# Kernel optimization log

Hardware: AMD Instinct MI355X
Metric: run time of the kernel (lower is better)

Reference implementation:

```python
import jax, jax.numpy as jnp
import numpy as np

ALPHA = 0.2      # LeakyReLU negative slope (alpha)
KNN = 5          # knn_num / cluster_num in get_center_1
M = 5            # m in get_dc
CC = 3           # cluster_centers
NEG = -9e15
EPS = 9e-15

def _pdist(x):
    sq = jnp.sum(x * x, axis=1)
    d2 = sq[:, None] + sq[None, :] - 2.0 * (x @ x.T)
    return jnp.sqrt(jnp.maximum(d2, 0.0))

def _cdist(x, c):
    d2 = jnp.sum(x * x, 1)[:, None] + jnp.sum(c * c, 1)[None, :] - 2.0 * (x @ c.T)
    return jnp.sqrt(jnp.maximum(d2, 0.0))

def _kmeans(x, k=CC, iters=10):
    # deterministic stand-in for sklearn KMeans(n_clusters=3, init='k-means++'):
    # farthest-point init + fixed Lloyd iterations
    c0 = x[0]
    d = jnp.sum((x - c0) ** 2, 1)
    c1 = x[jnp.argmax(d)]
    d = jnp.minimum(d, jnp.sum((x - c1) ** 2, 1))
    c2 = x[jnp.argmax(d)]
    centers = jnp.stack([c0, c1, c2])
    def step(c, _):
        assign = jnp.argmin(_cdist(x, c), axis=1)
        oh = jax.nn.one_hot(assign, k, dtype=x.dtype)
        newc = (oh.T @ x) / jnp.maximum(oh.sum(0), 1.0)[:, None]
        return newc, None
    centers, _ = jax.lax.scan(step, centers, None, length=iters)
    return centers

def _gravity(h):
    # get_center_1: fully built from detached tensors in the original -> stop_gradient
    x = jax.lax.stop_gradient(h)
    n = x.shape[0]
    z = _pdist(x)                                 # [n, n] pairwise distances
    negv, loc = jax.lax.top_k(-z, M + 1)          # M+1 smallest distances per row
    dc = jnp.mean(-negv[:, 1])                    # mean nearest-neighbor distance
    knn_idx = loc[:, 1:KNN + 1]                   # 5-NN (excluding self)
    rows = jnp.arange(n)[:, None]
    knn_vals = jnp.take_along_axis(z, knn_idx, axis=1)
    ori = jnp.zeros_like(z).at[rows, knn_idx].set(knn_vals)   # dists only at 5-NN
    nearest = jnp.take_along_axis(ori, loc[:, 1:2], axis=1)
    safe = jnp.where(ori != 0, ori, 1.0)
    ori = jnp.where(ori != 0, dc * nearest / (safe * safe), ori)
    # replicate the source's global flat-index mask (index = arange(size).reshape)
    flat = jnp.arange(n * n).reshape(n, n)
    mincol = jnp.min(jnp.argsort(ori, axis=1)[:, -KNN:], axis=1, keepdims=True)
    ori = jnp.where(flat >= mincol, 0.0, ori) - EPS
    centers = _kmeans(x)
    d1 = _cdist(x, centers)                       # [n, 3] node->center distances
    nearest1 = d1[:, 1:2]                         # cupy wrap: (i*3+1) % 3 == 1
    safe1 = jnp.where(d1 != 0, d1, 1.0)
    d1 = jnp.where(d1 != 0, dc * nearest1 / (safe1 * safe1), d1) - EPS
    z3 = jnp.full((CC, CC), NEG, dtype=x.dtype)
    top = jnp.concatenate([ori, d1], axis=1)
    bot = jnp.concatenate([d1.T, z3], axis=1)
    return jnp.concatenate([top, bot], axis=0)    # [(n+3), (n+3)]

def _forward(h, W, a, t1, t2):
    n, fin = h.shape
    fout = W.shape[1]
    Wh = h @ W
    s = Wh @ a[:fout] + (Wh @ a[fout:]).T         # [n, n]
    e = jnp.where(s > 0, s, ALPHA * s)            # LeakyReLU attention logits
    g = _gravity(h)
    att = jnp.concatenate([
        jnp.concatenate([e, t1], axis=1),
        jnp.concatenate([t2, jnp.zeros((CC, CC), h.dtype)], axis=1),
    ], axis=0)                                    # [(n+3), (n+3)]
    att = jax.nn.softmax(g @ att, axis=1)         # dropout omitted (eval mode)
    h_pad = jnp.concatenate([h, jnp.zeros((CC, fin), h.dtype)], axis=0)
    out = att @ (h_pad @ W)                       # [(n+3), fout]
    return jax.nn.elu(out)                        # concat=True

def setup_inputs():
    key = jax.random.key(0)
    k = jax.random.split(key, 5)
    N, FIN, FOUT = 4096, 512, 64
    gain = 1.414
    limW = gain * np.sqrt(6.0 / (FIN + FOUT))
    lima = gain * np.sqrt(6.0 / (2 * FOUT + 1))
    return {
        "h": jax.random.normal(k[0], (N, FIN), jnp.float32),
        "adj": jnp.zeros((N, N), jnp.float32),   # accepted but unused by forward
        "W": jax.random.uniform(k[1], (FIN, FOUT), jnp.float32, -limW, limW),
        "a": jax.random.uniform(k[2], (2 * FOUT, 1), jnp.float32, -lima, lima),
        "t1": jax.random.normal(k[3], (N, CC), jnp.float32),
        "t2": jax.random.normal(k[4], (CC, N), jnp.float32),
    }

def reference(h, adj, W, a, t1, t2):
    return _forward(h, W, a, t1, t2)
```

## Files before the change

### kernel.cpp

```cpp
#include <hip/hip_runtime.h>
#include <hip/hip_bf16.h>
#include <math.h>

#define NPTS 4096
#define FIN 512
#define FOUT 64
#define SCALE 4194304.0f
#define INVSCALE 2.384185791015625e-7f

typedef __attribute__((ext_vector_type(8))) short bf16x8;
typedef __attribute__((ext_vector_type(4))) float f32x4;
typedef unsigned long long ull;

static __device__ __forceinline__ unsigned short bfbits(float x) {
  __hip_bfloat16 b = __float2bfloat16(x);
  return *reinterpret_cast<unsigned short*>(&b);
}

static __device__ __forceinline__ float wsum64(float v) {
  #pragma unroll
  for (int mm = 1; mm < 64; mm <<= 1) v += __shfl_xor(v, mm);
  return v;
}

static __device__ __forceinline__ int aloadi(int* p) {
  return __hip_atomic_load(p, __ATOMIC_RELAXED, __HIP_MEMORY_SCOPE_AGENT);
}
static __device__ __forceinline__ ull aloadu(ull* p) {
  return __hip_atomic_load(p, __ATOMIC_RELAXED, __HIP_MEMORY_SCOPE_AGENT);
}

__global__ __launch_bounds__(256) void k_prep(const float* __restrict__ h,
    const float* __restrict__ W, __hip_bfloat16* __restrict__ xb,
    float* __restrict__ sq, int* __restrict__ m1, __hip_bfloat16* __restrict__ WbT,
    ull* __restrict__ accZ, int* __restrict__ cntZ, int* __restrict__ barZ) {
  int bid = blockIdx.x, t = threadIdx.x;
  if (bid >= 1026) {
    int idx = (bid - 1026) * 256 + t;
    #pragma unroll
    for (int s = 0; s < 10; ++s) accZ[s * 1536 + idx] = 0ull;
    if (idx < 40) cntZ[idx] = 0;
    if (idx < 32) barZ[idx] = 0;
    return;
  }
  if (bid >= 1024) {
    int base = (bid - 1024) * 16384;
    for (int rep = 0; rep < 64; ++rep) {
      int e = base + rep * 256 + t;
      int n = e >> 9, k = e & 511;
      WbT[e] = __float2bfloat16(W[k * FOUT + n]);
    }
    return;
  }
  int lane = t & 63, wid = t >> 6;
  int row = bid * 4 + wid;
  const float4* hr = (const float4*)(h + (size_t)row * FIN);
  float4 a = hr[lane], b = hr[64 + lane];
  ushort4 pa = { bfbits(a.x), bfbits(a.y), bfbits(a.z), bfbits(a.w) };
  ushort4 pb = { bfbits(b.x), bfbits(b.y), bfbits(b.z), bfbits(b.w) };
  *(ushort4*)(xb + (size_t)row * FIN + 4 * lane) = pa;
  *(ushort4*)(xb + (size_t)row * FIN + 256 + 4 * lane) = pb;
  float s = a.x*a.x + a.y*a.y + a.z*a.z + a.w*a.w
          + b.x*b.x + b.y*b.y + b.z*b.z + b.w*b.w;
  s = wsum64(s);
  if (lane == 0) { sq[row] = s; m1[row] = 0x7F800000; }
}

__device__ __forceinline__ void gram_role(const __hip_bfloat16* __restrict__ xb,
    const float* __restrict__ sq, int* __restrict__ m1, int gb, char* smem) {
  bool act = threadIdx.x < 256;
  int tid = threadIdx.x;
  int lane = tid & 63, wid = tid >> 6;
  int b = gb, I = 0;
  while (b >= 32 - I) { b -= 32 - I; ++I; }
  int J = I + b;
  char* As = smem;
  char* Bs = smem + 16384;

  int R0 = I * 128, C0 = J * 128;
  int rowBase = (wid >> 1) * 64;
  int colBase = (wid & 1) * 64;
  int lrow = lane & 15, hi = lane >> 4, rsub = hi * 4;

  f32x4 acc[4][4];
  #pragma unroll
  for (int p = 0; p < 4; ++p)
    #pragma unroll
    for (int q = 0; q < 4; ++q)
      acc[p][q] = (f32x4){0.f, 0.f, 0.f, 0.f};

  int srow = lane >> 3;
  int scol = ((lane & 7) ^ srow) * 8;
  const __hip_bfloat16* gA = xb + (size_t)(R0 + (wid & 3) * 32 + srow) * FIN + scol;
  const __hip_bfloat16* gB = xb + (size_t)(C0 + (wid & 3) * 32 + srow) * FIN + scol;
  char* lA = As + (wid & 3) * 4096;
  char* lB = Bs + (wid & 3) * 4096;
  int rdswz = (lrow & 7) << 4;

  for (int kt = 0; kt < 8; ++kt) {
    int K0 = kt * 64;
    if (act) {
      #pragma unroll
      for (int j = 0; j < 4; ++j) {
        __builtin_amdgcn_global_load_lds(
            (const __attribute__((address_space(1))) unsigned int*)(gA + (size_t)(8 * j) * FIN + K0),
            (__attribute__((address_space(3))) unsigned int*)(lA + j * 1024), 16, 0, 0);
        __builtin_amdgcn_global_load_lds(
            (const __attribute__((address_space(1))) unsigned int*)(gB + (size_t)(8 * j) * FIN + K0),
            (__attribute__((address_space(3))) unsigned int*)(lB + j * 1024), 16, 0, 0);
      }
    }
    __syncthreads();
    if (act) {
      #pragma unroll
      for (int s = 0; s < 2; ++s) {
        int k0b = s * 64;
        bf16x8 av[4], bw[4];
        #pragma unroll
        for (int f = 0; f < 4; ++f) {
          int arow = rowBase + f * 16 + lrow;
          av[f] = *(const bf16x8*)(As + arow * 128 + ((k0b + hi * 16) ^ rdswz));
          int brow = colBase + f * 16 + lrow;
          bw[f] = *(const bf16x8*)(Bs + brow * 128 + ((k0b + hi * 16) ^ rdswz));
        }
        #pragma unroll
        for (int fi = 0; fi < 4; ++fi)
          #pragma unroll
          for (int fj = 0; fj < 4; ++fj)
            acc[fi][fj] = __builtin_amdgcn_mfma_f32_16x16x32_bf16(av[fi], bw[fj], acc[fi][fj], 0, 0, 0);
      }
    }
    __syncthreads();
  }
  if (!act) return;

  int rowBaseG = R0 + rowBase, colBaseG = C0 + colBase;
  float sqr[16], sqc4[4];
  #pragma unroll
  for (int fi = 0; fi < 4; ++fi)
    #pragma unroll
    for (int rg = 0; rg < 4; ++rg)
      sqr[fi * 4 + rg] = sq[rowBaseG + fi * 16 + rsub + rg];
  #pragma unroll
  for (int fj = 0; fj < 4; ++fj) sqc4[fj] = sq[colBaseG + fj * 16 + lrow];

  float rmin[16], cmin[4];
  #pragma unroll
  for (int q = 0; q < 16; ++q) rmin[q] = INFINITY;
  #pragma unroll
  for (int q = 0; q < 4; ++q) cmin[q] = INFINITY;

  #pragma unroll
  for (int fi = 0; fi < 4; ++fi)
    #pragma unroll
    for (int fj = 0; fj < 4; ++fj)
      #pragma unroll
      for (int rg = 0; rg < 4; ++rg) {
        int r = rowBaseG + fi * 16 + rsub + rg;
        int c = colBaseG + fj * 16 + lrow;
        float d2 = sqr[fi * 4 + rg] + sqc4[fj] - 2.f * acc[fi][fj][rg];
        if (r == c) d2 = INFINITY;
        rmin[fi * 4 + rg] = fminf(rmin[fi * 4 + rg], d2);
        cmin[fj] = fminf(cmin[fj], d2);
      }

  #pragma unroll
  for (int mm = 1; mm < 16; mm <<= 1) {
    #pragma unroll
    for (int q = 0; q < 16; ++q) rmin[q] = fminf(rmin[q], __shfl_xor(rmin[q], mm));
  }
  if ((lane & 15) == 0) {
    #pragma unroll
    for (int q = 0; q < 16; ++q) {
      int r = rowBaseG + (q >> 2) * 16 + rsub + (q & 3);
      atomicMin(&m1[r], __float_as_int(rmin[q]));
    }
  }
  if (I != J) {
    #pragma unroll
    for (int mm = 16; mm < 64; mm <<= 1) {
      #pragma unroll
      for (int q = 0; q < 4; ++q) cmin[q] = fminf(cmin[q], __shfl_xor(cmin[q], mm));
    }
    if ((lane >> 4) == 0) {
      #pragma unroll
      for (int q = 0; q < 4; ++q)
        atomicMin(&m1[colBaseG + q * 16 + lane], __float_as_int(cmin[q]));
    }
  }
}

__device__ __forceinline__ void whmm_role(const __hip_bfloat16* __restrict__ xb,
    const __hip_bfloat16* __restrict__ WbT, float* __restrict__ Wh,
    __hip_bfloat16* __restrict__ WhbT, int wb) {
  int t = threadIdx.x, lane = t & 63, wid = t >> 6;
  int r16 = lane & 15, hi = lane >> 4;
  int rbase = wb * 128 + wid * 16;
  f32x4 acc[4];
  #pragma unroll
  for (int fn = 0; fn < 4; ++fn) acc[fn] = (f32x4){0.f, 0.f, 0.f, 0.f};
  const __hip_bfloat16* aP = xb + (size_t)(rbase + r16) * FIN + hi * 8;
  const __hip_bfloat16* bP[4];
  #pragma unroll
  for (int fn = 0; fn < 4; ++fn)
    bP[fn] = WbT + (size_t)(fn * 16 + r16) * FIN + hi * 8;
  #pragma unroll
  for (int kk = 0; kk < 16; ++kk) {
    bf16x8 a = *(const bf16x8*)(aP + kk * 32);
    #pragma unroll
    for (int fn = 0; fn < 4; ++fn) {
      bf16x8 bw = *(const bf16x8*)(bP[fn] + kk * 32);
      acc[fn] = __builtin_amdgcn_mfma_f32_16x16x32_bf16(a, bw, acc[fn], 0, 0, 0);
    }
  }
  #pragma unroll
  for (int fn = 0; fn < 4; ++fn)
    #pragma unroll
    for (int q = 0; q < 4; ++q) {
      float v = acc[fn][q];
      Wh[(size_t)(rbase + hi * 4 + q) * FOUT + fn * 16 + r16] = v;
      WhbT[(size_t)(fn * 16 + r16) * NPTS + rbase + hi * 4 + q] = __float2bfloat16(v);
    }
}

__device__ __forceinline__ void load_rows(const float* __restrict__ h, int rbase,
    int lane, float x[8][8]) {
  #pragma unroll
  for (int r = 0; r < 8; ++r) {
    const float4* xr = (const float4*)(h + (size_t)(rbase + r) * FIN);
    float4 u0 = xr[2 * lane], u1 = xr[2 * lane + 1];
    x[r][0]=u0.x; x[r][1]=u0.y; x[r][2]=u0.z; x[r][3]=u0.w;
    x[r][4]=u1.x; x[r][5]=u1.y; x[r][6]=u1.z; x[r][7]=u1.w;
  }
}

__device__ __forceinline__ void megabar(int* bar, int id) {
  __syncthreads();
  if (threadIdx.x == 0) {
    atomicAdd(&bar[id], 1);
    while (aloadi(&bar[id]) < 64) __builtin_amdgcn_s_sleep(2);
  }
  __syncthreads();
}

__global__ __launch_bounds__(512) void k_mega(
    const float* __restrict__ h, const float* __restrict__ sq,
    const __hip_bfloat16* __restrict__ xb, int* __restrict__ m1,
    const float* __restrict__ t2,
    int* __restrict__ bviA, int* __restrict__ biA,
    int* __restrict__ bviB, int* __restrict__ biB,
    float* __restrict__ tmpart, float* __restrict__ kvp, int* __restrict__ kip,
    ull* __restrict__ accum, int* __restrict__ cntAcc, int* __restrict__ bar,
    const __hip_bfloat16* __restrict__ WbT, float* __restrict__ Wh,
    __hip_bfloat16* __restrict__ WhbT) {
  __shared__ __align__(16) char smem[55552];
  int bid = blockIdx.x;
  if (bid >= 96) { gram_role(xb, sq, m1, bid - 96, smem); return; }
  if (bid >= 64) { whmm_role(xb, WbT, Wh, WhbT, bid - 64); return; }

  float* wsum  = (float*)smem;
  float* cents = (float*)(smem + 49152);
  float* rv    = (float*)(smem + 55296);
  int*   ri    = (int*)(smem + 55328);
  float* wcnt  = (float*)(smem + 55360);

  int t = threadIdx.x, lane = t & 63, wid = t >> 6, b = bid;
  int rbase = b * 64 + wid * 8;
  float x[8][8], sqr[8];
  load_rows(h, rbase, lane, x);
  #pragma unroll
  for (int r = 0; r < 8; ++r) sqr[r] = sq[rbase + r];

  float dloc[8];
  int b1, b2;

  {
    float cr[8];
    const float4* cp = (const float4*)h;
    float4 u0 = cp[2 * lane], u1 = cp[2 * lane + 1];
    cr[0]=u0.x;cr[1]=u0.y;cr[2]=u0.z;cr[3]=u0.w;cr[4]=u1.x;cr[5]=u1.y;cr[6]=u1.z;cr[7]=u1.w;
    float s0 = 0.f;
    #pragma unroll
    for (int q = 0; q < 8; ++q) s0 = fmaf(cr[q], cr[q], s0);
    float dd[8];
    #pragma unroll
    for (int r = 0; r < 8; ++r) dd[r] = 0.f;
    #pragma unroll
    for (int r = 0; r < 8; ++r)
      #pragma unroll
      for (int q = 0; q < 8; ++q) dd[r] = fmaf(x[r][q], cr[q], dd[r]);
    #pragma unroll
    for (int mm = 1; mm < 64; mm <<= 1) {
      s0 += __shfl_xor(s0, mm);
      #pragma unroll
      for (int r = 0; r < 8; ++r) dd[r] += __shfl_xor(dd[r], mm);
    }
    float bv = -1.f; int bi = 0;
    #pragma unroll
    for (int r = 0; r < 8; ++r) {
      float d = sqr[r] + s0 - 2.f * dd[r];
      dloc[r] = d;
      if (d > bv) { bv = d; bi = rbase + r; }
    }
    if (lane == 0) { rv[wid] = bv; ri[wid] = bi; }
  }
  __syncthreads();
  if (t == 0) {
    float vv = rv[0]; int ii = ri[0];
    for (int w = 1; w < 8; ++w)
      if (rv[w] > vv || (rv[w] == vv && ri[w] < ii)) { vv = rv[w]; ii = ri[w]; }
    atomicExch(&bviA[b], __float_as_int(vv));
    atomicExch(&biA[b], ii);
    atomicAdd(&bar[0], 1);
  }
  if (wid == 1) {
    #pragma unroll
    for (int c = 0; c < 3; ++c) {
      float m = fabsf(t2[c * NPTS + b * 64 + lane]);
      #pragma unroll
      for (int mm = 1; mm < 64; mm <<= 1) m = fmaxf(m, __shfl_xor(m, mm));
      if (lane == 0) tmpart[b * 3 + c] = m;
    }
  } else if (wid == 2) {
    int k = b * 64 + lane;
    float v = t2[k] + t2[NPTS + k] + t2[2 * NPTS + k];
    int ki = k;
    #pragma unroll
    for (int mm = 1; mm < 64; mm <<= 1) {
      float ov = __shfl_xor(v, mm); int oi = __shfl_xor(ki, mm);
      if (ov < v || (ov == v && oi < ki)) { v = ov; ki = oi; }
    }
    if (lane == 0) { kvp[b] = v; kip[b] = ki; }
  }
  if (t == 0) { while (aloadi(&bar[0]) < 64) __builtin_amdgcn_s_sleep(2); }
  __syncthreads();
  {
    float v = __int_as_float(aloadi(&bviA[lane]));
    int i = aloadi(&biA[lane]);
    #pragma unroll
    for (int mm = 1; mm < 64; mm <<= 1) {
      float ov = __shfl_xor(v, mm); int oi = __shfl_xor(i, mm);
      if (ov > v || (ov == v && oi < i)) { v = ov; i = oi; }
    }
    b1 = i;
  }

  {
    float cr[8];
    const float4* cp = (const float4*)(h + (size_t)b1 * FIN);
    float4 u0 = cp[2 * lane], u1 = cp[2 * lane + 1];
    cr[0]=u0.x;cr[1]=u0.y;cr[2]=u0.z;cr[3]=u0.w;cr[4]=u1.x;cr[5]=u1.y;cr[6]=u1.z;cr[7]=u1.w;
    float s0 = 0.f;
    #pragma unroll
    for (int q = 0; q < 8; ++q) s0 = fmaf(cr[q], cr[q], s0);
    float dd[8];
    #pragma unroll
    for (int r = 0; r < 8; ++r) dd[r] = 0.f;
    #pragma unroll
    for (int r = 0; r < 8; ++r)
      #pragma unroll
      for (int q = 0; q < 8; ++q) dd[r] = fmaf(x[r][q], cr[q], dd[r]);
    #pragma unroll
    for (int mm = 1; mm < 64; mm <<= 1) {
      s0 += __shfl_xor(s0, mm);
      #pragma unroll
      for (int r = 0; r < 8; ++r) dd[r] += __shfl_xor(dd[r], mm);
    }
    float bv = -1.f; int bi = 0;
    #pragma unroll
    for (int r = 0; r < 8; ++r) {
      float d = fminf(sqr[r] + s0 - 2.f * dd[r], dloc[r]);
      dloc[r] = d;
      if (d > bv) { bv = d; bi = rbase + r; }
    }
    if (lane == 0) { rv[wid] = bv; ri[wid] = bi; }
  }
  __syncthreads();
  if (t == 0) {
    float vv = rv[0]; int ii = ri[0];
    for (int w = 1; w < 8; ++w)
      if (rv[w] > vv || (rv[w] == vv && ri[w] < ii)) { vv = rv[w]; ii = ri[w]; }
    atomicExch(&bviB[b], __float_as_int(vv));
    atomicExch(&biB[b], ii);
    atomicAdd(&bar[1], 1);
    while (aloadi(&bar[1]) < 64) __builtin_amdgcn_s_sleep(2);
// ... 63 lines not shown
    #pragma unroll
    for (int mm = 1; mm < 64; mm <<= 1) {
      #pragma unroll
      for (int r = 0; r < 8; ++r) {
        d[r][0] += __shfl_xor(d[r][0], mm);
        d[r][1] += __shfl_xor(d[r][1], mm);
        d[r][2] += __shfl_xor(d[r][2], mm);
      }
    }
    float ps[3][8];
    #pragma unroll
    for (int c = 0; c < 3; ++c)
      #pragma unroll
      for (int q = 0; q < 8; ++q) ps[c][q] = 0.f;
    float cnt0 = 0.f, cnt1 = 0.f, cnt2 = 0.f;
    #pragma unroll
    for (int r = 0; r < 8; ++r) {
      float e0 = sqr[r] + s0 - 2.f * d[r][0];
      float e1 = sqr[r] + s1 - 2.f * d[r][1];
      float e2 = sqr[r] + s2 - 2.f * d[r][2];
      int bc = 0; float bd = e0;
      if (e1 < bd) { bd = e1; bc = 1; }
      if (e2 < bd) { bd = e2; bc = 2; }
      float f0 = bc == 0 ? 1.f : 0.f, f1 = bc == 1 ? 1.f : 0.f, f2 = bc == 2 ? 1.f : 0.f;
      #pragma unroll
      for (int q = 0; q < 8; ++q) {
        ps[0][q] = fmaf(f0, x[r][q], ps[0][q]);
        ps[1][q] = fmaf(f1, x[r][q], ps[1][q]);
        ps[2][q] = fmaf(f2, x[r][q], ps[2][q]);
      }
      cnt0 += f0; cnt1 += f1; cnt2 += f2;
    }
    #pragma unroll
    for (int c = 0; c < 3; ++c) {
      *(float4*)&wsum[wid * 1536 + c * 512 + 8 * lane]     = make_float4(ps[c][0], ps[c][1], ps[c][2], ps[c][3]);
      *(float4*)&wsum[wid * 1536 + c * 512 + 8 * lane + 4] = make_float4(ps[c][4], ps[c][5], ps[c][6], ps[c][7]);
    }
    if (lane == 0) { wcnt[wid * 3 + 0] = cnt0; wcnt[wid * 3 + 1] = cnt1; wcnt[wid * 3 + 2] = cnt2; }
    __syncthreads();
    ull* accO = accum + (size_t)it * 1536;
    for (int idx = t; idx < 1536; idx += 512) {
      float s = ((wsum[0*1536+idx] + wsum[1*1536+idx]) + (wsum[2*1536+idx] + wsum[3*1536+idx]))
              + ((wsum[4*1536+idx] + wsum[5*1536+idx]) + (wsum[6*1536+idx] + wsum[7*1536+idx]));
      long long q = llrintf(s * SCALE);
      atomicAdd(&accO[idx], (ull)q);
    }
    if (t < 3) {
      float s = 0.f;
      for (int w = 0; w < 8; ++w) s += wcnt[w * 3 + t];
      atomicAdd(&cntAcc[it * 4 + t], (int)(s + 0.5f));
    }
    if (it < 9) megabar(bar, 2 + it);
  }
}

__global__ __launch_bounds__(512) void k_mainC(
    const float* __restrict__ h, const float* __restrict__ sq,
    const float* __restrict__ t2, const __hip_bfloat16* __restrict__ WhbT,
    const float* __restrict__ Wh, const int* __restrict__ m1,
    const ull* __restrict__ accIn, const int* __restrict__ cntIn,
    const float* __restrict__ tmpart, const float* __restrict__ kvp,
    const int* __restrict__ kip, float* __restrict__ out) {
  __shared__ float t2s[3 * 4096];
  __shared__ float VcS[8][16][68];
  __shared__ float SpS[8][16];
  __shared__ float Mrow[16];
  __shared__ float a012[16][3];
  __shared__ float cents[1536];
  __shared__ float cntS[3];
  __shared__ float tmS[3];
  __shared__ float red[8];
  __shared__ int skstar;
  int t = threadIdx.x, lane = t & 63, wid = t >> 6;
  int R0 = blockIdx.x * 16;
  for (int idx = t; idx < 3072; idx += 512)
    ((f32x4*)t2s)[idx] = ((const f32x4*)t2)[idx];
  if (t < 3) {
    cntS[t] = fmaxf((float)cntIn[t], 1.f);
    float m = 0.f;
    for (int q = 0; q < 64; ++q) m = fmaxf(m, tmpart[q * 3 + t]);
    tmS[t] = m;
  }
  float sdc = 0.f;
  #pragma unroll
  for (int q = 0; q < 8; ++q)
    sdc += sqrtf(fmaxf(__int_as_float(m1[t + 512 * q]), 0.f));
  sdc = wsum64(sdc);
  if (lane == 0) red[wid] = sdc;
  __syncthreads();
  for (int idx = t; idx < 1536; idx += 512)
    cents[idx] = (float)(long long)accIn[idx] * INVSCALE / cntS[idx >> 9];
  __syncthreads();
  float dcv = (((red[0] + red[1]) + (red[2] + red[3])) + ((red[4] + red[5]) + (red[6] + red[7])))
            * (1.f / (float)NPTS);
  {
    float c0r[8], c1r[8], c2r[8];
    float4 u;
    u = *(const float4*)&cents[8 * lane];          c0r[0]=u.x;c0r[1]=u.y;c0r[2]=u.z;c0r[3]=u.w;
    u = *(const float4*)&cents[8 * lane + 4];      c0r[4]=u.x;c0r[5]=u.y;c0r[6]=u.z;c0r[7]=u.w;
    u = *(const float4*)&cents[512 + 8 * lane];    c1r[0]=u.x;c1r[1]=u.y;c1r[2]=u.z;c1r[3]=u.w;
    u = *(const float4*)&cents[512 + 8 * lane + 4];c1r[4]=u.x;c1r[5]=u.y;c1r[6]=u.z;c1r[7]=u.w;
    u = *(const float4*)&cents[1024 + 8 * lane];   c2r[0]=u.x;c2r[1]=u.y;c2r[2]=u.z;c2r[3]=u.w;
    u = *(const float4*)&cents[1024 + 8*lane + 4]; c2r[4]=u.x;c2r[5]=u.y;c2r[6]=u.z;c2r[7]=u.w;
    float s0 = 0.f, s1 = 0.f, s2 = 0.f;
    #pragma unroll
    for (int q = 0; q < 8; ++q) {
      s0 = fmaf(c0r[q], c0r[q], s0); s1 = fmaf(c1r[q], c1r[q], s1); s2 = fmaf(c2r[q], c2r[q], s2);
    }
    float xr2[2][8];
    #pragma unroll
    for (int rr = 0; rr < 2; ++rr) {
      int row = R0 + 2 * wid + rr;
      const float4* xr = (const float4*)(h + (size_t)row * FIN);
      float4 u0 = xr[2 * lane], u1 = xr[2 * lane + 1];
      xr2[rr][0]=u0.x; xr2[rr][1]=u0.y; xr2[rr][2]=u0.z; xr2[rr][3]=u0.w;
      xr2[rr][4]=u1.x; xr2[rr][5]=u1.y; xr2[rr][6]=u1.z; xr2[rr][7]=u1.w;
    }
    float dd[2][3];
    #pragma unroll
    for (int rr = 0; rr < 2; ++rr) { dd[rr][0]=0.f; dd[rr][1]=0.f; dd[rr][2]=0.f; }
    #pragma unroll
    for (int rr = 0; rr < 2; ++rr)
      #pragma unroll
      for (int q = 0; q < 8; ++q) {
        dd[rr][0] = fmaf(xr2[rr][q], c0r[q], dd[rr][0]);
        dd[rr][1] = fmaf(xr2[rr][q], c1r[q], dd[rr][1]);
        dd[rr][2] = fmaf(xr2[rr][q], c2r[q], dd[rr][2]);
      }
    #pragma unroll
    for (int mm = 1; mm < 64; mm <<= 1) {
      s0 += __shfl_xor(s0, mm); s1 += __shfl_xor(s1, mm); s2 += __shfl_xor(s2, mm);
      #pragma unroll
      for (int rr = 0; rr < 2; ++rr) {
        dd[rr][0] += __shfl_xor(dd[rr][0], mm);
        dd[rr][1] += __shfl_xor(dd[rr][1], mm);
        dd[rr][2] += __shfl_xor(dd[rr][2], mm);
      }
    }
    if (lane == 0) {
      #pragma unroll
      for (int rr = 0; rr < 2; ++rr) {
        int row = R0 + 2 * wid + rr;
        float sr = sq[row];
        float q0 = sqrtf(fmaxf(sr + s0 - 2.f * dd[rr][0], 0.f));
        float q1 = sqrtf(fmaxf(sr + s1 - 2.f * dd[rr][1], 0.f));
        float q2 = sqrtf(fmaxf(sr + s2 - 2.f * dd[rr][2], 0.f));
        float nr = q1;
        float a0 = (q0 != 0.f) ? (dcv * nr / (q0 * q0)) : 0.f;
        float a1 = (q1 != 0.f) ? (dcv * nr / (q1 * q1)) : 0.f;
        float a2 = (q2 != 0.f) ? (dcv * nr / (q2 * q2)) : 0.f;
        a012[2 * wid + rr][0] = a0; a012[2 * wid + rr][1] = a1; a012[2 * wid + rr][2] = a2;
        Mrow[2 * wid + rr] = fmaf(fabsf(a2), tmS[2], fmaf(fabsf(a1), tmS[1], fabsf(a0) * tmS[0]));
      }
    }
  }
  __syncthreads();
  int r16 = lane & 15, hi = lane >> 4;
  float a0 = a012[r16][0], a1 = a012[r16][1], a2 = a012[r16][2];
  float M = Mrow[r16];
  int K0 = wid * 512;
  f32x4 acc[4];
  #pragma unroll
  for (int fn = 0; fn < 4; ++fn) acc[fn] = (f32x4){0.f, 0.f, 0.f, 0.f};
  float Sp = 0.f;
  const __hip_bfloat16* bwB[4];
  #pragma unroll
  for (int fn = 0; fn < 4; ++fn)
    bwB[fn] = WhbT + (size_t)(fn * 16 + r16) * NPTS + K0 + hi * 8;

  for (int kst = 0; kst < 16; ++kst) {
    int kb = K0 + kst * 32 + hi * 8;
    f32x4 c0a = *(const f32x4*)&t2s[kb],        c0b = *(const f32x4*)&t2s[kb + 4];
    f32x4 c1a = *(const f32x4*)&t2s[4096 + kb], c1b = *(const f32x4*)&t2s[4096 + kb + 4];
    f32x4 c2a = *(const f32x4*)&t2s[8192 + kb], c2b = *(const f32x4*)&t2s[8192 + kb + 4];
    float pv[8];
    #pragma unroll
    for (int j = 0; j < 4; ++j) {
      float L  = fmaf(a0, c0a[j], fmaf(a1, c1a[j], fmaf(a2, c2a[j], -M)));
      pv[j] = __expf(L);
      float L2 = fmaf(a0, c0b[j], fmaf(a1, c1b[j], fmaf(a2, c2b[j], -M)));
      pv[4 + j] = __expf(L2);
    }
    Sp += ((pv[0] + pv[1]) + (pv[2] + pv[3])) + ((pv[4] + pv[5]) + (pv[6] + pv[7]));
    union { bf16x8 v; __hip_bfloat162 h2[4]; } pa;
    #pragma unroll
    for (int jj = 0; jj < 4; ++jj) {
      float2 f2; f2.x = pv[2 * jj]; f2.y = pv[2 * jj + 1];
      pa.h2[jj] = __float22bfloat162_rn(f2);
    }
    #pragma unroll
    for (int fn = 0; fn < 4; ++fn) {
      bf16x8 bw = *(const bf16x8*)(bwB[fn] + kst * 32);
      acc[fn] = __builtin_amdgcn_mfma_f32_16x16x32_bf16(pa.v, bw, acc[fn], 0, 0, 0);
    }
  }
  Sp += __shfl_xor(Sp, 16);
  Sp += __shfl_xor(Sp, 32);
  if (hi == 0) SpS[wid][r16] = Sp;
  #pragma unroll
  for (int fn = 0; fn < 4; ++fn)
    #pragma unroll
    for (int q = 0; q < 4; ++q)
      VcS[wid][hi * 4 + q][fn * 16 + r16] = acc[fn][q];
  __syncthreads();
  for (int e = t; e < 1024; e += 512) {
    int row = e >> 6, col = e & 63;
    float V = 0.f;
    #pragma unroll
    for (int w = 0; w < 8; ++w) V += VcS[w][row][col];
    float S = 3.f * __expf(-Mrow[row]);
    #pragma unroll
    for (int w = 0; w < 8; ++w) S += SpS[w][row];
    float o = V / S;
    out[(size_t)(R0 + row) * FOUT + col] = o > 0.f ? o : expm1f(o);
  }
  if (blockIdx.x == 0) {
    if (wid == 0) {
      float v = kvp[lane]; int i = kip[lane];
      #pragma unroll
      for (int mm = 1; mm < 64; mm <<= 1) {
        float ov = __shfl_xor(v, mm); int oi = __shfl_xor(i, mm);
        if (ov < v || (ov == v && oi < i)) { v = ov; i = oi; }
      }
      if (lane == 0) skstar = i;
    }
    __syncthreads();
    int kstar = skstar;
    if (t < 192) {
      int c = t >> 6, j = t & 63;
      float wv = Wh[(size_t)kstar * FOUT + j];
      out[(size_t)(NPTS + c) * FOUT + j] = wv > 0.f ? wv : expm1f(wv);
    }
  }
}

extern "C" void kernel_launch(void* const* d_in, const int* in_sizes, int n_in,
                              void* d_out, int out_size, void* d_ws, size_t ws_size,
                              hipStream_t stream) {
  const float* h  = (const float*)d_in[0];
  const float* W  = (const float*)d_in[2];
  const float* t2 = (const float*)d_in[5];
  float* out = (float*)d_out;

  char* ws = (char*)d_ws;
  __hip_bfloat16* xb = (__hip_bfloat16*)ws;
  float* F = (float*)(ws + (size_t)NPTS * FIN * 2);
  float* sq   = F + 0;
  int*   m1   = (int*)(F + 4096);
  float* Wh   = F + 32768;
  __hip_bfloat16* WhbT = (__hip_bfloat16*)(F + 1756672);
  __hip_bfloat16* WbT  = (__hip_bfloat16*)(F + 1887744);
  float* G = F + 1904128;
  int*   bviA   = (int*)(G + 0);
  int*   biA    = (int*)(G + 64);
  int*   bviB   = (int*)(G + 128);
  int*   biB    = (int*)(G + 192);
  float* tmpart = G + 384;
  float* kvp    = G + 576;
  int*   kip    = (int*)(G + 640);
  int*   bar    = (int*)(G + 704);
  ull*   accum  = (ull*)(G + 768);
  int*   cntAcc = (int*)(G + 768 + 30720);

  k_prep<<<1032, 256, 0, stream>>>(h, W, xb, sq, m1, WbT, accum, cntAcc, bar);
  k_mega<<<624, 512, 0, stream>>>(h, sq, xb, m1, t2, bviA, biA, bviB, biB,
                                  tmpart, kvp, kip, accum, cntAcc, bar, WbT, Wh, WhbT);
  k_mainC<<<256, 512, 0, stream>>>(h, sq, t2, WhbT, Wh, m1,
                                   (const ull*)(accum + 9 * 1536), (const int*)(cntAcc + 9 * 4),
                                   tmpart, kvp, kip, out);
}
```

Measured before the change: 136.5 us.

## Fuse final attention kernel into mega kernel via spin-wait counters

Removes the separate k_mainC launch. Its work now runs in the gram-role blocks of k_mega after each finishes its tile, gated by global atomic counters that the gram, Wh-GEMM and k-means roles increment when done. Producer writes become atomic exchanges so consumers see coherent values, and t2 is read straight from global memory instead of being staged in LDS. This saves a kernel launch and lets tail work overlap, but it risks spin-wait stalls, deadlock if blocks are not all co-resident, and extra atomic store traffic.

Measured after the change: 245.2 us. 1.8x slower.

```diff
diff --git a/kernel.cpp b/kernel.cpp
--- a/kernel.cpp
+++ b/kernel.cpp
@@ -23,11 +23,15 @@
   return v;
 }
 
-static __device__ __forceinline__ int aloadi(int* p) {
-  return __hip_atomic_load(p, __ATOMIC_RELAXED, __HIP_MEMORY_SCOPE_AGENT);
-}
-static __device__ __forceinline__ ull aloadu(ull* p) {
-  return __hip_atomic_load(p, __ATOMIC_RELAXED, __HIP_MEMORY_SCOPE_AGENT);
+static __device__ __forceinline__ int aloadi(const int* p) {
+  return __hip_atomic_load((int*)p, __ATOMIC_RELAXED, __HIP_MEMORY_SCOPE_AGENT);
+}
+static __device__ __forceinline__ ull aloadu(const ull* p) {
+  return __hip_atomic_load((ull*)p, __ATOMIC_RELAXED, __HIP_MEMORY_SCOPE_AGENT);
+}
+static __device__ __forceinline__ float aloadf(const float* p) {
+  int v = __hip_atomic_load((int*)p, __ATOMIC_RELAXED, __HIP_MEMORY_SCOPE_AGENT);
+  return __int_as_float(v);
 }
 
 __global__ __launch_bounds__(256) void k_prep(const float* __restrict__ h,
@@ -67,7 +71,8 @@
 }
 
 __device__ __forceinline__ void gram_role(const __hip_bfloat16* __restrict__ xb,
-    const float* __restrict__ sq, int* __restrict__ m1, int gb, char* smem) {
+    const float* __restrict__ sq, int* __restrict__ m1, int gb, char* smem,
+    int* __restrict__ bar) {
   bool act = threadIdx.x < 256;
   int tid = threadIdx.x;
   int lane = tid & 63, wid = tid >> 6;
@@ -132,67 +137,69 @@
     }
     __syncthreads();
   }
-  if (!act) return;
-
-  int rowBaseG = R0 + rowBase, colBaseG = C0 + colBase;
-  float sqr[16], sqc4[4];
-  #pragma unroll
-  for (int fi = 0; fi < 4; ++fi)
-    #pragma unroll
-    for (int rg = 0; rg < 4; ++rg)
-      sqr[fi * 4 + rg] = sq[rowBaseG + fi * 16 + rsub + rg];
-  #pragma unroll
-  for (int fj = 0; fj < 4; ++fj) sqc4[fj] = sq[colBaseG + fj * 16 + lrow];
-
-  float rmin[16], cmin[4];
-  #pragma unroll
-  for (int q = 0; q < 16; ++q) rmin[q] = INFINITY;
-  #pragma unroll
-  for (int q = 0; q < 4; ++q) cmin[q] = INFINITY;
-
-  #pragma unroll
-  for (int fi = 0; fi < 4; ++fi)
-    #pragma unroll
-    for (int fj = 0; fj < 4; ++fj)
-      #pragma unroll
-      for (int rg = 0; rg < 4; ++rg) {
-        int r = rowBaseG + fi * 16 + rsub + rg;
-        int c = colBaseG + fj * 16 + lrow;
-        float d2 = sqr[fi * 4 + rg] + sqc4[fj] - 2.f * acc[fi][fj][rg];
-        if (r == c) d2 = INFINITY;
-        rmin[fi * 4 + rg] = fminf(rmin[fi * 4 + rg], d2);
-        cmin[fj] = fminf(cmin[fj], d2);
-      }
-
-  #pragma unroll
-  for (int mm = 1; mm < 16; mm <<= 1) {
-    #pragma unroll
-    for (int q = 0; q < 16; ++q) rmin[q] = fminf(rmin[q], __shfl_xor(rmin[q], mm));
-  }
-  if ((lane & 15) == 0) {
-    #pragma unroll
-    for (int q = 0; q < 16; ++q) {
-      int r = rowBaseG + (q >> 2) * 16 + rsub + (q & 3);
-      atomicMin(&m1[r], __float_as_int(rmin[q]));
-    }
-  }
-  if (I != J) {
-    #pragma unroll
-    for (int mm = 16; mm < 64; mm <<= 1) {
-      #pragma unroll
-      for (int q = 0; q < 4; ++q) cmin[q] = fminf(cmin[q], __shfl_xor(cmin[q], mm));
-    }
-    if ((lane >> 4) == 0) {
-      #pragma unroll
-      for (int q = 0; q < 4; ++q)
-        atomicMin(&m1[colBaseG + q * 16 + lane], __float_as_int(cmin[q]));
-    }
-  }
+  if (act) {
+    int rowBaseG = R0 + rowBase, colBaseG = C0 + colBase;
+    float sqr[16], sqc4[4];
+    #pragma unroll
+    for (int fi = 0; fi < 4; ++fi)
+      #pragma unroll
+      for (int rg = 0; rg < 4; ++rg)
+        sqr[fi * 4 + rg] = sq[rowBaseG + fi * 16 + rsub + rg];
+    #pragma unroll
+    for (int fj = 0; fj < 4; ++fj) sqc4[fj] = sq[colBaseG + fj * 16 + lrow];
+
+    float rmin[16], cmin[4];
+    #pragma unroll
+    for (int q = 0; q < 16; ++q) rmin[q] = INFINITY;
+    #pragma unroll
+    for (int q = 0; q < 4; ++q) cmin[q] = INFINITY;
+
+    #pragma unroll
+    for (int fi = 0; fi < 4; ++fi)
+      #pragma unroll
+      for (int fj = 0; fj < 4; ++fj)
+        #pragma unroll
+        for (int rg = 0; rg < 4; ++rg) {
+          int r = rowBaseG + fi * 16 + rsub + rg;
+          int c = colBaseG + fj * 16 + lrow;
+          float d2 = sqr[fi * 4 + rg] + sqc4[fj] - 2.f * acc[fi][fj][rg];
+          if (r == c) d2 = INFINITY;
+          rmin[fi * 4 + rg] = fminf(rmin[fi * 4 + rg], d2);
+          cmin[fj] = fminf(cmin[fj], d2);
+        }
+
+    #pragma unroll
+    for (int mm = 1; mm < 16; mm <<= 1) {
+      #pragma unroll
+      for (int q = 0; q < 16; ++q) rmin[q] = fminf(rmin[q], __shfl_xor(rmin[q], mm));
+    }
+    if ((lane & 15) == 0) {
+      #pragma unroll
+      for (int q = 0; q < 16; ++q) {
+        int r = rowBaseG + (q >> 2) * 16 + rsub + (q & 3);
+        atomicMin(&m1[r], __float_as_int(rmin[q]));
+      }
+    }
+    if (I != J) {
+      #pragma unroll
+      for (int mm = 16; mm < 64; mm <<= 1) {
+        #pragma unroll
+        for (int q = 0; q < 4; ++q) cmin[q] = fminf(cmin[q], __shfl_xor(cmin[q], mm));
+      }
+      if ((lane >> 4) == 0) {
+        #pragma unroll
+        for (int q = 0; q < 4; ++q)
+          atomicMin(&m1[colBaseG + q * 16 + lane], __float_as_int(cmin[q]));
+      }
+    }
+  }
+  __syncthreads();
+  if (tid == 0) atomicAdd(&bar[12], 1);
 }
 
 __device__ __forceinline__ void whmm_role(const __hip_bfloat16* __restrict__ xb,
     const __hip_bfloat16* __restrict__ WbT, float* __restrict__ Wh,
-    __hip_bfloat16* __restrict__ WhbT, int wb) {
+    __hip_bfloat16* __restrict__ WhbT, int wb, int* __restrict__ bar) {
   int t = threadIdx.x, lane = t & 63, wid = t >> 6;
   int r16 = lane & 15, hi = lane >> 4;
   int rbase = wb * 128 + wid * 16;
@@ -213,14 +220,21 @@
       acc[fn] = __builtin_amdgcn_mfma_f32_16x16x32_bf16(a, bw, acc[fn], 0, 0, 0);
     }
   }
-  #pragma unroll
-  for (int fn = 0; fn < 4; ++fn)
-    #pragma unroll
-    for (int q = 0; q < 4; ++q) {
-      float v = acc[fn][q];
-      Wh[(size_t)(rbase + hi * 4 + q) * FOUT + fn * 16 + r16] = v;
-      WhbT[(size_t)(fn * 16 + r16) * NPTS + rbase + hi * 4 + q] = __float2bfloat16(v);
-    }
+  int* WhI = (int*)Wh;
+  #pragma unroll
+  for (int fn = 0; fn < 4; ++fn) {
+    #pragma unroll
+    for (int q = 0; q < 4; ++q)
+      atomicExch(&WhI[(size_t)(rbase + hi * 4 + q) * FOUT + fn * 16 + r16],
+                 __float_as_int(acc[fn][q]));
+    unsigned p01 = (unsigned)bfbits(acc[fn][0]) | ((unsigned)bfbits(acc[fn][1]) << 16);
+    unsigned p23 = (unsigned)bfbits(acc[fn][2]) | ((unsigned)bfbits(acc[fn][3]) << 16);
+    unsigned* WT = (unsigned*)(WhbT + (size_t)(fn * 16 + r16) * NPTS + rbase + hi * 4);
+    atomicExch(&WT[0], p01);
+    atomicExch(&WT[1], p23);
+  }
+  __syncthreads();
+  if (t == 0) atomicAdd(&bar[13], 1);
 }
 
 __device__ __forceinline__ void load_rows(const float* __restrict__ h, int rbase,
@@ -243,7 +257,194 @@
   __syncthreads();
 }
 
-__global__ __launch_bounds__(512) void k_mega(
+__device__ void mainc_role(const float* __restrict__ h, const float* __restrict__ sq,
+    const float* __restrict__ t2, const __hip_bfloat16* __restrict__ WhbT,
+    const float* __restrict__ Wh, const int* __restrict__ m1,
+    const ull* __restrict__ acc9, const int* __restrict__ cnt9,
+    const float* __restrict__ tmpart, const float* __restrict__ kvp,
+    const int* __restrict__ kip, int* __restrict__ bar,
+    float* __restrict__ out, int g, char* smem) {
+  float* VcS  = (float*)smem;
+  float* cents = (float*)(smem + 34816);
+  float* SpS  = (float*)(smem + 40960);
+  float* Mrow = (float*)(smem + 41472);
+  float* a012 = (float*)(smem + 41536);
+  float* tmS  = (float*)(smem + 41728);
+  float* red  = (float*)(smem + 41744);
+  int*  skst  = (int*)(smem + 41776);
+  float* cntS = (float*)(smem + 41780);
+
+  int t = threadIdx.x, lane = t & 63, wid = t >> 6;
+  int R0 = g * 16;
+  if (t == 0) {
+    while (aloadi(&bar[13]) < 32)  __builtin_amdgcn_s_sleep(4);
+    while (aloadi(&bar[12]) < 528) __builtin_amdgcn_s_sleep(4);
+    while (aloadi(&bar[11]) < 64)  __builtin_amdgcn_s_sleep(4);
+  }
+  __syncthreads();
+
+  if (t < 3) {
+    cntS[t] = fmaxf((float)aloadi(&cnt9[t]), 1.f);
+    float m = 0.f;
+    for (int q = 0; q < 64; ++q) m = fmaxf(m, aloadf(&tmpart[q * 3 + t]));
+    tmS[t] = m;
+  }
+  float sdc = 0.f;
+  #pragma unroll
+  for (int q = 0; q < 8; ++q)
+    sdc += sqrtf(fmaxf(__int_as_float(aloadi(&m1[t + 512 * q])), 0.f));
+  sdc = wsum64(sdc);
+  if (lane == 0) red[wid] = sdc;
+  __syncthreads();
+  for (int idx = t; idx < 1536; idx += 512)
+    cents[idx] = (float)(long long)aloadu(&acc9[idx]) * INVSCALE / cntS[idx >> 9];
+  __syncthreads();
+  float dcv = (((red[0] + red[1]) + (red[2] + red[3])) + ((red[4] + red[5]) + (red[6] + red[7])))
+            * (1.f / (float)NPTS);
+  {
+    float c0r[8], c1r[8], c2r[8];
+    float4 u;
+    u = *(const float4*)&cents[8 * lane];          c0r[0]=u.x;c0r[1]=u.y;c0r[2]=u.z;c0r[3]=u.w;
+    u = *(const float4*)&cents[8 * lane + 4];      c0r[4]=u.x;c0r[5]=u.y;c0r[6]=u.z;c0r[7]=u.w;
+    u = *(const float4*)&cents[512 + 8 * lane];    c1r[0]=u.x;c1r[1]=u.y;c1r[2]=u.z;c1r[3]=u.w;
+    u = *(const float4*)&cents[512 + 8 * lane + 4];c1r[4]=u.x;c1r[5]=u.y;c1r[6]=u.z;c1r[7]=u.w;
+    u = *(const float4*)&cents[1024 + 8 * lane];   c2r[0]=u.x;c2r[1]=u.y;c2r[2]=u.z;c2r[3]=u.w;
+    u = *(const float4*)&cents[1024 + 8*lane + 4]; c2r[4]=u.x;c2r[5]=u.y;c2r[6]=u.z;c2r[7]=u.w;
+    float s0 = 0.f, s1 = 0.f, s2 = 0.f;
+    #pragma unroll
+    for (int q = 0; q < 8; ++q) {
+      s0 = fmaf(c0r[q], c0r[q], s0); s1 = fmaf(c1r[q], c1r[q], s1); s2 = fmaf(c2r[q], c2r[q], s2);
+    }
+    float xr2[2][8];
+    #pragma unroll
+    for (int rr = 0; rr < 2; ++rr) {
+      int row = R0 + 2 * wid + rr;
+      const float4* xr = (const float4*)(h + (size_t)row * FIN);
+      float4 u0 = xr[2 * lane], u1 = xr[2 * lane + 1];
+      xr2[rr][0]=u0.x; xr2[rr][1]=u0.y; xr2[rr][2]=u0.z; xr2[rr][3]=u0.w;
+      xr2[rr][4]=u1.x; xr2[rr][5]=u1.y; xr2[rr][6]=u1.z; xr2[rr][7]=u1.w;
+    }
+    float dd[2][3];
+    #pragma unroll
+    for (int rr = 0; rr < 2; ++rr) { dd[rr][0]=0.f; dd[rr][1]=0.f; dd[rr][2]=0.f; }
+    #pragma unroll
+    for (int rr = 0; rr < 2; ++rr)
+      #pragma unroll
+      for (int q = 0; q < 8; ++q) {
+        dd[rr][0] = fmaf(xr2[rr][q], c0r[q], dd[rr][0]);
+        dd[rr][1] = fmaf(xr2[rr][q], c1r[q], dd[rr][1]);
+        dd[rr][2] = fmaf(xr2[rr][q], c2r[q], dd[rr][2]);
+      }
+    #pragma unroll
+    for (int mm = 1; mm < 64; mm <<= 1) {
+      s0 += __shfl_xor(s0, mm); s1 += __shfl_xor(s1, mm); s2 += __shfl_xor(s2, mm);
+      #pragma unroll
+      for (int rr = 0; rr < 2; ++rr) {
+        dd[rr][0] += __shfl_xor(dd[rr][0], mm);
+        dd[rr][1] += __shfl_xor(dd[rr][1], mm);
+        dd[rr][2] += __shfl_xor(dd[rr][2], mm);
+      }
+    }
+    if (lane == 0) {
+      #pragma unroll
+      for (int rr = 0; rr < 2; ++rr) {
+        int row = R0 + 2 * wid + rr;
+        float sr = sq[row];
+        float q0 = sqrtf(fmaxf(sr + s0 - 2.f * dd[rr][0], 0.f));
+        float q1 = sqrtf(fmaxf(sr + s1 - 2.f * dd[rr][1], 0.f));
+        float q2 = sqrtf(fmaxf(sr + s2 - 2.f * dd[rr][2], 0.f));
+        float nr = q1;
+        float a0 = (q0 != 0.f) ? (dcv * nr / (q0 * q0)) : 0.f;
+        float a1 = (q1 != 0.f) ? (dcv * nr / (q1 * q1)) : 0.f;
+        float a2 = (q2 != 0.f) ? (dcv * nr / (q2 * q2)) : 0.f;
+        a012[(2 * wid + rr) * 3 + 0] = a0;
+        a012[(2 * wid + rr) * 3 + 1] = a1;
+        a012[(2 * wid + rr) * 3 + 2] = a2;
+        Mrow[2 * wid + rr] = fmaf(fabsf(a2), tmS[2], fmaf(fabsf(a1), tmS[1], fabsf(a0) * tmS[0]));
+      }
+    }
+  }
+  __syncthreads();
+  int r16 = lane & 15, hi = lane >> 4;
+  float a0 = a012[r16 * 3 + 0], a1 = a012[r16 * 3 + 1], a2 = a012[r16 * 3 + 2];
+  float M = Mrow[r16];
+  int K0 = wid * 512;
+  f32x4 acc[4];
+  #pragma unroll
+  for (int fn = 0; fn < 4; ++fn) acc[fn] = (f32x4){0.f, 0.f, 0.f, 0.f};
+  float Sp = 0.f;
+  const __hip_bfloat16* bwB[4];
+  #pragma unroll
+  for (int fn = 0; fn < 4; ++fn)
+    bwB[fn] = WhbT + (size_t)(fn * 16 + r16) * NPTS + K0 + hi * 8;
+
+  for (int kst = 0; kst < 16; ++kst) {
+    int kb = K0 + kst * 32 + hi * 8;
+    f32x4 c0a = *(const f32x4*)&t2[kb],        c0b = *(const f32x4*)&t2[kb + 4];
+    f32x4 c1a = *(const f32x4*)&t2[4096 + kb], c1b = *(const f32x4*)&t2[4096 + kb + 4];
+    f32x4 c2a = *(const f32x4*)&t2[8192 + kb], c2b = *(const f32x4*)&t2[8192 + kb + 4];
+    float pv[8];
+    #pragma unroll
+    for (int j = 0; j < 4; ++j) {
+      float L  = fmaf(a0, c0a[j], fmaf(a1, c1a[j], fmaf(a2, c2a[j], -M)));
+      pv[j] = __expf(L);
+      float L2 = fmaf(a0, c0b[j], fmaf(a1, c1b[j], fmaf(a2, c2b[j], -M)));
+      pv[4 + j] = __expf(L2);
+    }
+    Sp += ((pv[0] + pv[1]) + (pv[2] + pv[3])) + ((pv[4] + pv[5]) + (pv[6] + pv[7]));
+    union { bf16x8 v; __hip_bfloat162 h2[4]; } pa;
+    #pragma unroll
+    for (int jj = 0; jj < 4; ++jj) {
+      float2 f2; f2.x = pv[2 * jj]; f2.y = pv[2 * jj + 1];
+      pa.h2[jj] = __float22bfloat162_rn(f2);
+    }
+    #pragma unroll
+    for (int fn = 0; fn < 4; ++fn) {
+      bf16x8 bw = *(const bf16x8*)(bwB[fn] + kst * 32);
+      acc[fn] = __builtin_amdgcn_mfma_f32_16x16x32_bf16(pa.v, bw, acc[fn], 0, 0, 0);
+    }
+  }
+  Sp += __shfl_xor(Sp, 16);
+  Sp += __shfl_xor(Sp, 32);
+  if (hi == 0) SpS[wid * 16 + r16] = Sp;
+  #pragma unroll
+  for (int fn = 0; fn < 4; ++fn)
+    #pragma unroll
+    for (int q = 0; q < 4; ++q)
+      VcS[(wid * 16 + hi * 4 + q) * 68 + fn * 16 + r16] = acc[fn][q];
+  __syncthreads();
+  for (int e = t; e < 1024; e += 512) {
+    int row = e >> 6, col = e & 63;
+    float V = 0.f;
+    #pragma unroll
+    for (int w = 0; w < 8; ++w) V += VcS[(w * 16 + row) * 68 + col];
+    float S = 3.f * __expf(-Mrow[row]);
+    #pragma unroll
+    for (int w = 0; w < 8; ++w) S += SpS[w * 16 + row];
+    float o = V / S;
+    out[(size_t)(R0 + row) * FOUT + col] = o > 0.f ? o : expm1f(o);
+  }
+  if (g == 0) {
+    if (wid == 0) {
+      float v = aloadf(&kvp[lane]); int i = aloadi(&kip[lane]);
+      #pragma unroll
+      for (int mm = 1; mm < 64; mm <<= 1) {
+        float ov = __shfl_xor(v, mm); int oi = __shfl_xor(i, mm);
+        if (ov < v || (ov == v && oi < i)) { v = ov; i = oi; }
+      }
+      if (lane == 0) skst[0] = i;
+    }
+    __syncthreads();
+    int kstar = skst[0];
+    if (t < 192) {
+      int c = t >> 6, j = t & 63;
+      float wv = aloadf(&Wh[(size_t)kstar * FOUT + j]);
+      out[(size_t)(NPTS + c) * FOUT + j] = wv > 0.f ? wv : expm1f(wv);
+    }
+  }
+}
+
+__global__ __launch_bounds__(512, 4) void k_mega(
     const float* __restrict__ h, const float* __restrict__ sq,
     const __hip_bfloat16* __restrict__ xb, int* __restrict__ m1,
     const float* __restrict__ t2,
@@ -252,11 +453,18 @@
     float* __restrict__ tmpart, float* __restrict__ kvp, int* __restrict__ kip,
     ull* __restrict__ accum, int* __restrict__ cntAcc, int* __restrict__ bar,
     const __hip_bfloat16* __restrict__ WbT, float* __restrict__ Wh,
-    __hip_bfloat16* __restrict__ WhbT) {
+    __hip_bfloat16* __restrict__ WhbT, float* __restrict__ out) {
   __shared__ __align__(16) char smem[55552];
   int bid = blockIdx.x;
-  if (bid >= 96) { gram_role(xb, sq, m1, bid - 96, smem); return; }
-  if (bid >= 64) { whmm_role(xb, WbT, Wh, WhbT, bid - 64); return; }
+  if (bid >= 96) {
+    gram_role(xb, sq, m1, bid - 96, smem, bar);
+    int g = bid - 96;
+    if (g < 256)
+      mainc_role(h, sq, t2, WhbT, Wh, m1, accum + 9 * 1536, cntAcc + 9 * 4,
+                 tmpart, kvp, kip, bar, out, g, smem);
+    return;
+  }
+  if (bid >= 64) { whmm_role(xb, WbT, Wh, WhbT, bid - 64, bar); return; }
 
   float* wsum  = (float*)smem;
   float* cents = (float*)(smem + 49152);
@@ -319,7 +527,7 @@
       float m = fabsf(t2[c * NPTS + b * 64 + lane]);
       #pragma unroll
       for (int mm = 1; mm < 64; mm <<= 1) m = fmaxf(m, __shfl_xor(m, mm));
-      if (lane == 0) tmpart[b * 3 + c] = m;
+      if (lane == 0) atomicExch((int*)&tmpart[b * 3 + c], __float_as_int(m));
     }
   } else if (wid == 2) {
     int k = b * 64 + lane;
@@ -330,7 +538,7 @@
       float ov = __shfl_xor(v, mm); int oi = __shfl_xor(ki, mm);
       if (ov < v || (ov == v && oi < ki)) { v = ov; ki = oi; }
     }
-    if (lane == 0) { kvp[b] = v; kip[b] = ki; }
+    if (lane == 0) { atomicExch((int*)&kvp[b], __float_as_int(v)); atomicExch(&kip[b], ki); }
   }
   if (t == 0) { while (aloadi(&bar[0]) < 64) __builtin_amdgcn_s_sleep(2); }
   __syncthreads();
@@ -500,186 +708,8 @@
     }
     if (it < 9) megabar(bar, 2 + it);
   }
-}
-
-__global__ __launch_bounds__(512) void k_mainC(
-    const float* __restrict__ h, const float* __restrict__ sq,
-    const float* __restrict__ t2, const __hip_bfloat16* __restrict__ WhbT,
-    const float* __restrict__ Wh, const int* __restrict__ m1,
-    const ull* __restrict__ accIn, const int* __restrict__ cntIn,
-    const float* __restrict__ tmpart, const float* __restrict__ kvp,
-    const int* __restrict__ kip, float* __restrict__ out) {
-  __shared__ float t2s[3 * 4096];
-  __shared__ float VcS[8][16][68];
-  __shared__ float SpS[8][16];
-  __shared__ float Mrow[16];
-  __shared__ float a012[16][3];
-  __shared__ float cents[1536];
-  __shared__ float cntS[3];
-  __shared__ float tmS[3];
-  __shared__ float red[8];
-  __shared__ int skstar;
-  int t = threadIdx.x, lane = t & 63, wid = t >> 6;
-  int R0 = blockIdx.x * 16;
-  for (int idx = t; idx < 3072; idx += 512)
-    ((f32x4*)t2s)[idx] = ((const f32x4*)t2)[idx];
-  if (t < 3) {
-    cntS[t] = fmaxf((float)cntIn[t], 1.f);
-    float m = 0.f;
-    for (int q = 0; q < 64; ++q) m = fmaxf(m, tmpart[q * 3 + t]);
-    tmS[t] = m;
-  }
-  float sdc = 0.f;
-  #pragma unroll
-  for (int q = 0; q < 8; ++q)
-    sdc += sqrtf(fmaxf(__int_as_float(m1[t + 512 * q]), 0.f));
-  sdc = wsum64(sdc);
-  if (lane == 0) red[wid] = sdc;
-  __syncthreads();
-  for (int idx = t; idx < 1536; idx += 512)
-    cents[idx] = (float)(long long)accIn[idx] * INVSCALE / cntS[idx >> 9];
-  __syncthreads();
-  float dcv = (((red[0] + red[1]) + (red[2] + red[3])) + ((red[4] + red[5]) + (red[6] + red[7])))
-            * (1.f / (float)NPTS);
-  {
-    float c0r[8], c1r[8], c2r[8];
-    float4 u;
-    u = *(const float4*)&cents[8 * lane];          c0r[0]=u.x;c0r[1]=u.y;c0r[2]=u.z;c0r[3]=u.w;
-    u = *(const float4*)&cents[8 * lane + 4];      c0r[4]=u.x;c0r[5]=u.y;c0r[6]=u.z;c0r[7]=u.w;
-    u = *(const float4*)&cents[512 + 8 * lane];    c1r[0]=u.x;c1r[1]=u.y;c1r[2]=u.z;c1r[3]=u.w;
-    u = *(const float4*)&cents[512 + 8 * lane + 4];c1r[4]=u.x;c1r[5]=u.y;c1r[6]=u.z;c1r[7]=u.w;
-    u = *(const float4*)&cents[1024 + 8 * lane];   c2r[0]=u.x;c2r[1]=u.y;c2r[2]=u.z;c2r[3]=u.w;
-    u = *(const float4*)&cents[1024 + 8*lane + 4]; c2r[4]=u.x;c2r[5]=u.y;c2r[6]=u.z;c2r[7]=u.w;
-    float s0 = 0.f, s1 = 0.f, s2 = 0.f;
-    #pragma unroll
-    for (int q = 0; q < 8; ++q) {
-      s0 = fmaf(c0r[q], c0r[q], s0); s1 = fmaf(c1r[q], c1r[q], s1); s2 = fmaf(c2r[q], c2r[q], s2);
-    }
-    float xr2[2][8];
-    #pragma unroll
-    for (int rr = 0; rr < 2; ++rr) {
-      int row = R0 + 2 * wid + rr;
-      const float4* xr = (const float4*)(h + (size_t)row * FIN);
-      float4 u0 = xr[2 * lane], u1 = xr[2 * lane + 1];
-      xr2[rr][0]=u0.x; xr2[rr][1]=u0.y; xr2[rr][2]=u0.z; xr2[rr][3]=u0.w;
-      xr2[rr][4]=u1.x; xr2[rr][5]=u1.y; xr2[rr][6]=u1.z; xr2[rr][7]=u1.w;
-    }
-    float dd[2][3];
-    #pragma unroll
-    for (int rr = 0; rr < 2; ++rr) { dd[rr][0]=0.f; dd[rr][1]=0.f; dd[rr][2]=0.f; }
-    #pragma unroll
-    for (int rr = 0; rr < 2; ++rr)
-      #pragma unroll
-      for (int q = 0; q < 8; ++q) {
-        dd[rr][0] = fmaf(xr2[rr][q], c0r[q], dd[rr][0]);
-        dd[rr][1] = fmaf(xr2[rr][q], c1r[q], dd[rr][1]);
-        dd[rr][2] = fmaf(xr2[rr][q], c2r[q], dd[rr][2]);
-      }
-    #pragma unroll
-    for (int mm = 1; mm < 64; mm <<= 1) {
-      s0 += __shfl_xor(s0, mm); s1 += __shfl_xor(s1, mm); s2 += __shfl_xor(s2, mm);
-      #pragma unroll
-      for (int rr = 0; rr < 2; ++rr) {
-        dd[rr][0] += __shfl_xor(dd[rr][0], mm);
-        dd[rr][1] += __shfl_xor(dd[rr][1], mm);
-        dd[rr][2] += __shfl_xor(dd[rr][2], mm);
-      }
-    }
-    if (lane == 0) {
-      #pragma unroll
-      for (int rr = 0; rr < 2; ++rr) {
-        int row = R0 + 2 * wid + rr;
-        float sr = sq[row];
-        float q0 = sqrtf(fmaxf(sr + s0 - 2.f * dd[rr][0], 0.f));
-        float q1 = sqrtf(fmaxf(sr + s1 - 2.f * dd[rr][1], 0.f));
-        float q2 = sqrtf(fmaxf(sr + s2 - 2.f * dd[rr][2], 0.f));
-        float nr = q1;
-        float a0 = (q0 != 0.f) ? (dcv * nr / (q0 * q0)) : 0.f;
-        float a1 = (q1 != 0.f) ? (dcv * nr / (q1 * q1)) : 0.f;
-        float a2 = (q2 != 0.f) ? (dcv * nr / (q2 * q2)) : 0.f;
-        a012[2 * wid + rr][0] = a0; a012[2 * wid + rr][1] = a1; a012[2 * wid + rr][2] = a2;
-        Mrow[2 * wid + rr] = fmaf(fabsf(a2), tmS[2], fmaf(fabsf(a1), tmS[1], fabsf(a0) * tmS[0]));
-      }
-    }
-  }
-  __syncthreads();
-  int r16 = lane & 15, hi = lane >> 4;
-  float a0 = a012[r16][0], a1 = a012[r16][1], a2 = a012[r16][2];
-  float M = Mrow[r16];
-  int K0 = wid * 512;
-  f32x4 acc[4];
-  #pragma unroll
-  for (int fn = 0; fn < 4; ++fn) acc[fn] = (f32x4){0.f, 0.f, 0.f, 0.f};
-  float Sp = 0.f;
-  const __hip_bfloat16* bwB[4];
-  #pragma unroll
-  for (int fn = 0; fn < 4; ++fn)
-    bwB[fn] = WhbT + (size_t)(fn * 16 + r16) * NPTS + K0 + hi * 8;
-
-  for (int kst = 0; kst < 16; ++kst) {
-    int kb = K0 + kst * 32 + hi * 8;
-    f32x4 c0a = *(const f32x4*)&t2s[kb],        c0b = *(const f32x4*)&t2s[kb + 4];
-    f32x4 c1a = *(const f32x4*)&t2s[4096 + kb], c1b = *(const f32x4*)&t2s[4096 + kb + 4];
-    f32x4 c2a = *(const f32x4*)&t2s[8192 + kb], c2b = *(const f32x4*)&t2s[8192 + kb + 4];
-    float pv[8];
-    #pragma unroll
-    for (int j = 0; j < 4; ++j) {
-      float L  = fmaf(a0, c0a[j], fmaf(a1, c1a[j], fmaf(a2, c2a[j], -M)));
-      pv[j] = __expf(L);
-      float L2 = fmaf(a0, c0b[j], fmaf(a1, c1b[j], fmaf(a2, c2b[j], -M)));
-      pv[4 + j] = __expf(L2);
-    }
-    Sp += ((pv[0] + pv[1]) + (pv[2] + pv[3])) + ((pv[4] + pv[5]) + (pv[6] + pv[7]));
-    union { bf16x8 v; __hip_bfloat162 h2[4]; } pa;
-    #pragma unroll
-    for (int jj = 0; jj < 4; ++jj) {
-      float2 f2; f2.x = pv[2 * jj]; f2.y = pv[2 * jj + 1];
-      pa.h2[jj] = __float22bfloat162_rn(f2);
-    }
-    #pragma unroll
-    for (int fn = 0; fn < 4; ++fn) {
-      bf16x8 bw = *(const bf16x8*)(bwB[fn] + kst * 32);
-      acc[fn] = __builtin_amdgcn_mfma_f32_16x16x32_bf16(pa.v, bw, acc[fn], 0, 0, 0);
-    }
-  }
-  Sp += __shfl_xor(Sp, 16);
-  Sp += __shfl_xor(Sp, 32);
-  if (hi == 0) SpS[wid][r16] = Sp;
-  #pragma unroll
-  for (int fn = 0; fn < 4; ++fn)
-    #pragma unroll
-    for (int q = 0; q < 4; ++q)
-      VcS[wid][hi * 4 + q][fn * 16 + r16] = acc[fn][q];
-  __syncthreads();
-  for (int e = t; e < 1024; e += 512) {
-    int row = e >> 6, col = e & 63;
-    float V = 0.f;
-    #pragma unroll
-    for (int w = 0; w < 8; ++w) V += VcS[w][row][col];
-    float S = 3.f * __expf(-Mrow[row]);
-    #pragma unroll
-    for (int w = 0; w < 8; ++w) S += SpS[w][row];
-    float o = V / S;
-    out[(size_t)(R0 + row) * FOUT + col] = o > 0.f ? o : expm1f(o);
-  }
-  if (blockIdx.x == 0) {
-    if (wid == 0) {
-      float v = kvp[lane]; int i = kip[lane];
-      #pragma unroll
-      for (int mm = 1; mm < 64; mm <<= 1) {
-        float ov = __shfl_xor(v, mm); int oi = __shfl_xor(i, mm);
-        if (ov < v || (ov == v && oi < i)) { v = ov; i = oi; }
-      }
-      if (lane == 0) skstar = i;
-    }
-    __syncthreads();
-    int kstar = skstar;
-    if (t < 192) {
-      int c = t >> 6, j = t & 63;
-      float wv = Wh[(size_t)kstar * FOUT + j];
-      out[(size_t)(NPTS + c) * FOUT + j] = wv > 0.f ? wv : expm1f(wv);
-    }
-  }
+  __syncthreads();
+  if (t == 0) atomicAdd(&bar[11], 1);
 }
 
 extern "C" void kernel_launch(void* const* d_in, const int* in_sizes, int n_in,
@@ -712,8 +742,5 @@
 
   k_prep<<<1032, 256, 0, stream>>>(h, W, xb, sq, m1, WbT, accum, cntAcc, bar);
   k_mega<<<624, 512, 0, stream>>>(h, sq, xb, m1, t2, bviA, biA, bviB, biB,
-                                  tmpart, kvp, kip, accum, cntAcc, bar, WbT, Wh, WhbT);
-  k_mainC<<<256, 512, 0, stream>>>(h, sq, t2, WhbT, Wh, m1,
-                                   (const ull*)(accum + 9 * 1536), (const int*)(cntAcc + 9 * 4),
-                                   tmpart, kvp, kip, out);
-}
+                                  tmpart, kvp, kip, accum, cntAcc, bar, WbT, Wh, WhbT, out);
+}
```
